# Kernel tuning notes

Measured on AMD Instinct MI355X. Metric: run time of the kernel, lower is better.

Reference implementation:

```python
import jax, jax.numpy as jnp
import numpy as np

BEV_H, BEV_W = 496, 432  # cfg.bevshape

def mish(x):
    return x * jnp.tanh(jax.nn.softplus(x))

def ln(x, g, b, eps=1e-5):
    m = jnp.mean(x, axis=-1, keepdims=True)
    v = jnp.mean((x - m) ** 2, axis=-1, keepdims=True)
    return (x - m) * jax.lax.rsqrt(v + eps) * g + b

def fel(x, W, g, b):
    # FELayer: Linear(bias=False) -> LayerNorm -> Mish
    return mish(ln(x @ W.T, g, b))

def setup_inputs() -> dict:
    key = jax.random.key(0)
    ks = iter(jax.random.split(key, 48))
    Nv, P, Cin, Cv, Nb = 16000, 32, 10, 64, 16000
    inp = {}
    inp['voxels'] = jax.random.normal(next(ks), (Nv, P, Cin), jnp.float32)
    inp['voxelmask'] = jax.random.bernoulli(next(ks), 0.7, (Nv, P, 1)).astype(jnp.float32)
    inp['bevsidx'] = jax.random.randint(next(ks), (Nb, 64), 0, Nv, dtype=jnp.int32)
    flat = jax.random.choice(next(ks), BEV_H * BEV_W, (Nb,), replace=False)
    inp['bevcoors'] = jnp.stack([flat // BEV_W, flat % BEV_W], axis=1).astype(jnp.int32)
    inp['bevmask'] = jax.random.bernoulli(next(ks), 0.8, (Nb, 1, 1)).astype(jnp.float32)
    def w(shape):
        return jax.random.normal(next(ks), shape, jnp.float32) * 0.05
    for i, cin in zip((1, 2, 3, 4), (Cin, Cv, Cv, Cv)):
        inp[f'vfe{i}_W'] = w((Cv, cin))
        inp[f'vfe{i}_g'] = jnp.ones((Cv,), jnp.float32)
        inp[f'vfe{i}_b'] = jnp.zeros((Cv,), jnp.float32)
    inp['bfe1_W'] = w((16, Cv, Cv));  inp['bfe1_g'] = jnp.ones((16, Cv));  inp['bfe1_b'] = jnp.zeros((16, Cv))
    inp['bfe2a_W'] = w((16, 8, Cv)); inp['bfe2a_g'] = jnp.ones((16, 8));  inp['bfe2a_b'] = jnp.zeros((16, 8))
    inp['bfe2b_W'] = w((16, 8, 32)); inp['bfe2b_g'] = jnp.ones((16, 8));  inp['bfe2b_b'] = jnp.zeros((16, 8))
    inp['bfe3_W'] = w((128, 128));   inp['bfe3_g'] = jnp.ones((128,));   inp['bfe3_b'] = jnp.zeros((128,))
    return inp

def reference(voxels, voxelmask, bevsidx, bevcoors, bevmask,
              vfe1_W, vfe1_g, vfe1_b, vfe2_W, vfe2_g, vfe2_b,
              vfe3_W, vfe3_g, vfe3_b, vfe4_W, vfe4_g, vfe4_b,
              bfe1_W, bfe1_g, bfe1_b, bfe2a_W, bfe2a_g, bfe2a_b,
              bfe2b_W, bfe2b_g, bfe2b_b, bfe3_W, bfe3_g, bfe3_b):
    # voxel feature encoder with masked residual
    x1 = fel(voxels, vfe1_W, vfe1_g, vfe1_b)            # [Nv, P, 64]
    x2 = fel(x1, vfe2_W, vfe2_g, vfe2_b) * voxelmask
    x3 = fel(x2, vfe3_W, vfe3_g, vfe3_b)
    x4 = fel(x3, vfe4_W, vfe4_g, vfe4_b) * voxelmask + x2
    voxelwise = jnp.max(x4, axis=1)                     # [Nv, 64]
    # gather 64 voxels per BEV cell
    bevs = voxelwise[bevsidx]                           # [Nb, 64 voxels, 64 ch]
    x0 = jnp.transpose(bevs, (0, 2, 1))                 # [Nb, 64 ch, 64 voxels]
    Nb = x0.shape[0]
    xg = x0.reshape(Nb, 16, 4, 64)                      # 16 branches of 4 channel-rows
    # bfe1_k (vectorized over the 16 branches) + bev mask
    h = mish(ln(jnp.einsum('ngpc,goc->ngpo', xg, bfe1_W), bfe1_g[:, None, :], bfe1_b[:, None, :]))
    h = h * bevmask[:, None]                            # bevmask [Nb,1,1] -> broadcast
    # bfe2_k: NormalFELayer(in_points=4, in=64, out=8)
    h = mish(ln(jnp.einsum('ngpc,goc->ngpo', h, bfe2a_W), bfe2a_g[:, None, :], bfe2a_b[:, None, :]))
    h = h.reshape(Nb, 16, 32)
    h = mish(ln(jnp.einsum('ngc,goc->ngo', h, bfe2b_W), bfe2b_g, bfe2b_b))  # [Nb,16,8]
    x17 = h.reshape(Nb, 128)                            # cat of 16 branches
    x18 = fel(x17, bfe3_W, bfe3_g, bfe3_b)
    x19 = fel(x18, bfe3_W, bfe3_g, bfe3_b) + x17        # same bfe3 applied twice + residual
    bevmap = jnp.zeros((BEV_H, BEV_W, 128), jnp.float32).at[bevcoors[:, 0], bevcoors[:, 1]].set(x19)
    return jnp.transpose(bevmap, (2, 1, 0))             # [128, W, H]
```

## Files before the change

kernel.cpp:

```cpp
#include <hip/hip_runtime.h>
#include <math.h>

constexpr int NV  = 16000;
constexpr int P   = 32;
constexpr int CIN = 10;
constexpr int CV  = 64;
constexpr int NB  = 16000;
constexpr int BEV_H = 496, BEV_W = 432;
constexpr int HW = BEV_H * BEV_W;
constexpr float EPS = 1e-5f;

typedef __attribute__((ext_vector_type(8))) short short8_t;
typedef __attribute__((ext_vector_type(4))) short short4_t;
typedef __attribute__((ext_vector_type(4))) float fx4;
typedef __attribute__((ext_vector_type(2))) float f32x2;

__device__ __forceinline__ float mish(float x) {
  float e = __expf(fminf(x, 15.f));
  float u = 1.f + e;
  float d = fmaf(u, u, 1.f);
  float r = __builtin_amdgcn_rcpf(d);
  return fmaf(-2.f * x, r, x);
}

__device__ __forceinline__ f32x2 mish2(f32x2 x) {
  f32x2 xc = __builtin_elementwise_min(x, (f32x2){15.f, 15.f});
  f32x2 e  = { __expf(xc[0]), __expf(xc[1]) };
  f32x2 u  = e + (f32x2){1.f, 1.f};
  f32x2 d  = __builtin_elementwise_fma(u, u, (f32x2){1.f, 1.f});
  f32x2 r  = { __builtin_amdgcn_rcpf(d[0]), __builtin_amdgcn_rcpf(d[1]) };
  f32x2 m2x = x * (f32x2){-2.f, -2.f};
  return __builtin_elementwise_fma(m2x, r, x);
}
__device__ __forceinline__ f32x2 ln2(f32x2 a, f32x2 rs, f32x2 msv, f32x2 go, f32x2 bo) {
  return __builtin_elementwise_fma(__builtin_elementwise_fma(a, rs, msv), go, bo);
}

__device__ __forceinline__ short f2bf(float f) {
  unsigned u = __builtin_bit_cast(unsigned, f);
  u += 0x7FFF + ((u >> 16) & 1);
  return (short)(u >> 16);
}
__device__ __forceinline__ float bf2f(short s) {
  unsigned u = ((unsigned)(unsigned short)s) << 16;
  return __builtin_bit_cast(float, u);
}
__device__ __forceinline__ short8_t pack8(const float* t) {
  short8_t s;
#pragma unroll
  for (int j = 0; j < 8; ++j) s[j] = f2bf(t[j]);
  return s;
}

__device__ __forceinline__ unsigned bfpair(float a, float b) {
  unsigned au = __builtin_bit_cast(unsigned, a) + 0x8000u;
  unsigned bu = __builtin_bit_cast(unsigned, b) + 0x8000u;
  return __builtin_amdgcn_perm(bu, au, 0x07060302u);
}
__device__ __forceinline__ unsigned hipack(float a, float b, float& la, float& lb) {
  unsigned ua = (__builtin_bit_cast(unsigned, a) + 0x8000u) & 0xFFFF0000u;
  unsigned ub = (__builtin_bit_cast(unsigned, b) + 0x8000u) & 0xFFFF0000u;
  la = a - __builtin_bit_cast(float, ua);
  lb = b - __builtin_bit_cast(float, ub);
  return __builtin_amdgcn_perm(ub, ua, 0x07060302u);
}

constexpr int VFE_BLOCKS  = NV / 16;
constexpr int PACK_BLOCKS = 208;

__global__ __launch_bounds__(512, 4) void vfe_pack_kernel(
    const float* __restrict__ voxels, const float* __restrict__ vmask,
    const float* __restrict__ W1, const float* __restrict__ g1, const float* __restrict__ b1,
    const float* __restrict__ W2, const float* __restrict__ g2, const float* __restrict__ b2,
    const float* __restrict__ W3, const float* __restrict__ g3, const float* __restrict__ b3,
    const float* __restrict__ W4, const float* __restrict__ g4, const float* __restrict__ b4,
    unsigned short* __restrict__ voxelwise,
    const float* __restrict__ bW1, const float* __restrict__ bW2a,
    const float* __restrict__ bW2b, const float* __restrict__ bW3,
    const int* __restrict__ bevcoors,
    short* __restrict__ w1h, short* __restrict__ w2ah, short* __restrict__ w2bh,
    short* __restrict__ w3h, short* __restrict__ w3l,
    int* __restrict__ invmap)
{
  __shared__ short wlds[28 * 512];
  __shared__ short actb[8][16 * 72];
  __shared__ float gblds[512];
  __shared__ unsigned short pairbuf[2][4][4][64];

  const int tid = threadIdx.x;

  if (blockIdx.x >= VFE_BLOCKS) {
    int i = (blockIdx.x - VFE_BLOCKS) * 512 + tid;
    if (i < NB) {
      int2 hw2 = *(const int2*)&bevcoors[i * 2];
      invmap[hw2.y * BEV_H + hw2.x] = i;
    }
    if (i < 65536) {
      w1h[i] = f2bf(bW1[i]);
    } else if (i < 81920) {
      int j = i - 65536;
      int g = j >> 10, o = (j >> 6) & 15, c = j & 63;
      float v = (o < 8) ? bW2a[(g * 8 + o) * 64 + c] : 0.f;
      w2ah[j] = f2bf(v);
    } else if (i < 90112) {
      int k = i - 81920;
      int g = k >> 9, o = (k >> 5) & 15, c = k & 31;
      float v = (o < 8) ? bW2b[(g * 8 + o) * 32 + c] : 0.f;
      w2bh[k] = f2bf(v);
    } else if (i < 106496) {
      int j = i - 90112;
      float v = bW3[j];
      short h = f2bf(v);
      w3h[j] = h; w3l[j] = f2bf(v - bf2f(h));
    }
    return;
  }

  const int lane = tid & 63;
  const int w    = tid >> 6;
  const int pair = w >> 1;
  const int h    = w & 1;
  const int p    = lane & 15;
  const int q    = lane >> 4;
  const int gw   = blockIdx.x * 4 + pair;

  {
    int region = tid >> 6, off = tid & 63;
    const float* src =
        region == 0 ? g1 : region == 1 ? b1 :
        region == 2 ? g2 : region == 3 ? b2 :
        region == 4 ? g3 : region == 5 ? b3 :
        region == 6 ? g4 : b4;
    gblds[tid] = src[off];
  }
  for (int s = w; s < 28; s += 8) {
    float t[8];
    if (s < 4) {
      const int f = s;
#pragma unroll
      for (int j = 0; j < 8; ++j) {
        int c = 8 * q + j;
        t[j] = (c < CIN) ? W1[(p + 16 * f) * CIN + c] : 0.f;
      }
    } else {
      const int l = (s - 4) >> 3, rem = (s - 4) & 7, ch = rem >> 2, f = rem & 3;
      const float* Wl = (l == 0) ? W2 : (l == 1) ? W3 : W4;
      const float* src = Wl + (p + 16 * f) * CV + 32 * ch + 8 * q;
#pragma unroll
      for (int j = 0; j < 8; ++j) t[j] = src[j];
    }
    *(short8_t*)&wlds[s * 512 + lane * 8] = pack8(t);
  }
  __syncthreads();

  short* mybuf = &actb[w][0];
  const fx4 zacc = {0.f, 0.f, 0.f, 0.f};
  const int srcLane = ((lane >> 2) & 3) * 16 + (((lane >> 4) & 3) << 2) + (lane & 3);

  for (int i = 0; i < 4; ++i) {
    const int v = gw * 4 + i;
    const int ptbase = v * 32 + h * 16;
    const float m = vmask[ptbase + p];
    const f32x2 mv = {m, m};
    f32x2 x2r2[8];
    float cur[16];

    {
      const float* xrow = voxels + (size_t)(ptbase + p) * CIN;
      float t[8] = {0.f, 0.f, 0.f, 0.f, 0.f, 0.f, 0.f, 0.f};
      if (q == 0) {
        float2 a = *(const float2*)(xrow + 0);
        float2 b = *(const float2*)(xrow + 2);
        float2 c = *(const float2*)(xrow + 4);
        float2 d = *(const float2*)(xrow + 6);
        t[0] = a.x; t[1] = a.y; t[2] = b.x; t[3] = b.y;
        t[4] = c.x; t[5] = c.y; t[6] = d.x; t[7] = d.y;
      } else if (q == 1) {
        float2 a = *(const float2*)(xrow + 8);
        t[0] = a.x; t[1] = a.y;
      }
      uint4 bu = make_uint4(bfpair(t[0], t[1]), bfpair(t[2], t[3]),
                            bfpair(t[4], t[5]), bfpair(t[6], t[7]));
      short8_t bfrag = __builtin_bit_cast(short8_t, bu);
      fx4 acc[4];
#pragma unroll
      for (int f = 0; f < 4; ++f) {
        short8_t af = *(short8_t*)&wlds[f * 512 + lane * 8];
        acc[f] = __builtin_amdgcn_mfma_f32_16x16x32_bf16(af, bfrag, zacc, 0, 0, 0);
      }
      f32x2 s1v = {0.f, 0.f}, s2v = {0.f, 0.f};
#pragma unroll
      for (int f = 0; f < 4; ++f) {
        f32x2 a01 = __builtin_shufflevector(acc[f], acc[f], 0, 1);
        f32x2 a23 = __builtin_shufflevector(acc[f], acc[f], 2, 3);
        s1v = s1v + a01 + a23;
        s2v = __builtin_elementwise_fma(a01, a01, s2v);
        s2v = __builtin_elementwise_fma(a23, a23, s2v);
      }
      float s1 = s1v[0] + s1v[1], s2 = s2v[0] + s2v[1];
      s1 += __shfl_xor(s1, 16); s1 += __shfl_xor(s1, 32);
      s2 += __shfl_xor(s2, 16); s2 += __shfl_xor(s2, 32);
      float mean = s1 * (1.f / 64.f);
      float rstd = rsqrtf(fmaf(-mean, mean, s2 * (1.f / 64.f)) + EPS);
      float ms = -mean * rstd;
      const f32x2 rs = {rstd, rstd}, msv = {ms, ms};
#pragma unroll
      for (int f = 0; f < 4; ++f) {
        float4 gv = *(const float4*)&gblds[16 * f + 4 * q];
        float4 bv = *(const float4*)&gblds[64 + 16 * f + 4 * q];
        f32x2 a01 = __builtin_shufflevector(acc[f], acc[f], 0, 1);
        f32x2 a23 = __builtin_shufflevector(acc[f], acc[f], 2, 3);
        f32x2 o01 = mish2(ln2(a01, rs, msv, (f32x2){gv.x, gv.y}, (f32x2){bv.x, bv.y}));
        f32x2 o23 = mish2(ln2(a23, rs, msv, (f32x2){gv.z, gv.w}, (f32x2){bv.z, bv.w}));
        *(uint2*)&mybuf[p * 72 + 4 * q + 16 * f] =
            make_uint2(bfpair(o01[0], o01[1]), bfpair(o23[0], o23[1]));
      }
    }

#pragma unroll 1
    for (int l = 0; l < 3; ++l) {
      short8_t bf0 = *(short8_t*)&mybuf[p * 72 + 8 * q];
      short8_t bf1 = *(short8_t*)&mybuf[p * 72 + 8 * q + 32];
      fx4 acc[4];
#pragma unroll
      for (int f = 0; f < 4; ++f) {
        short8_t a0 = *(short8_t*)&wlds[(4 + l * 8 + f) * 512 + lane * 8];
        short8_t a1 = *(short8_t*)&wlds[(4 + l * 8 + 4 + f) * 512 + lane * 8];
        fx4 a = __builtin_amdgcn_mfma_f32_16x16x32_bf16(a0, bf0, zacc, 0, 0, 0);
        acc[f] = __builtin_amdgcn_mfma_f32_16x16x32_bf16(a1, bf1, a, 0, 0, 0);
      }
      f32x2 s1v = {0.f, 0.f}, s2v = {0.f, 0.f};
#pragma unroll
      for (int f = 0; f < 4; ++f) {
        f32x2 a01 = __builtin_shufflevector(acc[f], acc[f], 0, 1);
        f32x2 a23 = __builtin_shufflevector(acc[f], acc[f], 2, 3);
        s1v = s1v + a01 + a23;
        s2v = __builtin_elementwise_fma(a01, a01, s2v);
        s2v = __builtin_elementwise_fma(a23, a23, s2v);
      }
      float s1 = s1v[0] + s1v[1], s2 = s2v[0] + s2v[1];
      s1 += __shfl_xor(s1, 16); s1 += __shfl_xor(s1, 32);
      s2 += __shfl_xor(s2, 16); s2 += __shfl_xor(s2, 32);
      float mean = s1 * (1.f / 64.f);
      float rstd = rsqrtf(fmaf(-mean, mean, s2 * (1.f / 64.f)) + EPS);
      float ms = -mean * rstd;
      const f32x2 rs = {rstd, rstd}, msv = {ms, ms};
      const int gbbase = (l + 1) * 128;
#pragma unroll
      for (int f = 0; f < 4; ++f) {
        float4 gv = *(const float4*)&gblds[gbbase + 16 * f + 4 * q];
        float4 bv = *(const float4*)&gblds[gbbase + 64 + 16 * f + 4 * q];
        f32x2 go01 = {gv.x, gv.y}, go23 = {gv.z, gv.w};
        f32x2 bo01 = {bv.x, bv.y}, bo23 = {bv.z, bv.w};
        f32x2 a01 = __builtin_shufflevector(acc[f], acc[f], 0, 1);
        f32x2 a23 = __builtin_shufflevector(acc[f], acc[f], 2, 3);
        if (l == 0) {
          f32x2 o01 = mish2(ln2(a01, rs, msv, go01, bo01)) * mv;
          f32x2 o23 = mish2(ln2(a23, rs, msv, go23, bo23)) * mv;
          x2r2[2 * f] = o01; x2r2[2 * f + 1] = o23;
          *(uint2*)&mybuf[p * 72 + 4 * q + 16 * f] =
              make_uint2(bfpair(o01[0], o01[1]), bfpair(o23[0], o23[1]));
        } else if (l == 1) {
          f32x2 o01 = mish2(ln2(a01, rs, msv, go01, bo01));
          f32x2 o23 = mish2(ln2(a23, rs, msv, go23, bo23));
          *(uint2*)&mybuf[p * 72 + 4 * q + 16 * f] =
              make_uint2(bfpair(o01[0], o01[1]), bfpair(o23[0], o23[1]));
        } else {
          f32x2 c01 = __builtin_elementwise_fma(
              mish2(ln2(a01, rs, msv, go01, bo01)), mv, x2r2[2 * f]);
          f32x2 c23 = __builtin_elementwise_fma(
              mish2(ln2(a23, rs, msv, go23, bo23)), mv, x2r2[2 * f + 1]);
          cur[f * 4 + 0] = c01[0]; cur[f * 4 + 1] = c01[1];
          cur[f * 4 + 2] = c23[0]; cur[f * 4 + 3] = c23[1];
        }
      }
    }

#pragma unroll
    for (int t = 0; t < 8; ++t) {
      float send = (lane & 8) ? cur[t] : cur[t + 8];
      float got  = __shfl_xor(send, 8);
      float mine = (lane & 8) ? cur[t + 8] : cur[t];
      cur[t] = fmaxf(mine, got);
    }
#pragma unroll
    for (int t = 0; t < 4; ++t) {
      float send = (lane & 4) ? cur[t] : cur[t + 4];
      float got  = __shfl_xor(send, 4);
      float mine = (lane & 4) ? cur[t + 4] : cur[t];
      cur[t] = fmaxf(mine, got);
    }
#pragma unroll
    for (int t = 0; t < 2; ++t) {
      float send = (lane & 2) ? cur[t] : cur[t + 2];
      float got  = __shfl_xor(send, 2);
      float mine = (lane & 2) ? cur[t + 2] : cur[t];
      cur[t] = fmaxf(mine, got);
    }
    {
      float send = (lane & 1) ? cur[0] : cur[1];
      float got  = __shfl_xor(send, 1);
      float mine = (lane & 1) ? cur[1] : cur[0];
      cur[0] = fmaxf(mine, got);
    }
    float hm = __shfl(cur[0], srcLane);
    unsigned hu = __builtin_bit_cast(unsigned, hm) + 0x8000u;
    pairbuf[h][pair][i][lane] = (unsigned short)(hu >> 16);
  }

  __syncthreads();

  if (h == 0) {
#pragma unroll
    for (int i = 0; i < 4; ++i) {
      const int v = gw * 4 + i;
      float a = bf2f((short)pairbuf[0][pair][i][lane]);
      float b = bf2f((short)pairbuf[1][pair][i][lane]);
      float vmaxv = fmaxf(a, b);
      voxelwise[v * 64 + lane] =
          (unsigned short)(__builtin_bit_cast(unsigned, vmaxv) >> 16);
    }
  }
}

constexpr int XS_CELL = 64 * 64 + 16;
constexpr int ACT_OFF = 4 * XS_CELL;
constexpr int ACT_WS  = 16 * 72;
constexpr int GB_OFF  = ACT_OFF + 8 * ACT_WS;
constexpr int GB_FLOATS = 2560;
constexpr int SMEM_SHORTS = GB_OFF + 2 * (GB_FLOATS + 4 * 132);

__device__ __forceinline__ uint2 gather_transpose(uint2 u2, int bit0, int bit1) {
  float a0 = __builtin_bit_cast(float, u2.x << 16);
  float a1 = __builtin_bit_cast(float, u2.x & 0xFFFF0000u);
  float a2 = __builtin_bit_cast(float, u2.y << 16);
  float a3 = __builtin_bit_cast(float, u2.y & 0xFFFF0000u);
  float gv0 = bit0 ? a0 : a1, gv1 = bit0 ? a2 : a3;
  float r0 = __shfl_xor(gv0, 4), r1 = __shfl_xor(gv1, 4);
  float c0 = bit0 ? r0 : a0, c1 = bit0 ? a1 : r0;
  float c2 = bit0 ? r1 : a2, c3 = bit0 ? a3 : r1;
  float h0 = bit1 ? c0 : c2, h1 = bit1 ? c1 : c3;
  float s0 = __shfl_xor(h0, 8), s1 = __shfl_xor(h1, 8);
  float d0 = bit1 ? s0 : c0, d1 = bit1 ? s1 : c1;
  float d2 = bit1 ? c2 : s0, d3 = bit1 ? c3 : s1;
  return make_uint2(bfpair(d0, d1), bfpair(d2, d3));
}

__global__ __launch_bounds__(512, 3) void bfe12_mfma10_kernel(
    const unsigned short* __restrict__ voxelwise, const int* __restrict__ bevsidx,
    const float* __restrict__ bevmask,
    const short* __restrict__ w1h,
    const float* __restrict__ g1, const float* __restrict__ b1,
    const short* __restrict__ w2ah,
    const float* __restrict__ g2a, const float* __restrict__ b2a,
    const short* __restrict__ w2bh,
    const float* __restrict__ g2b, const float* __restrict__ b2b,
    float* __restrict__ x17buf)
{
  __shared__ short sm[SMEM_SHORTS];
  float* gbf  = (float*)&sm[GB_OFF];
  float* x17f = gbf + GB_FLOATS;

  const int tid  = threadIdx.x;
  const int lane = tid & 63;
  const int w    = tid >> 6;
  const int r15  = lane & 15;
  const int q    = lane >> 4;
  const int cellbase = blockIdx.x * 4;

  const int chq   = lane & 3;
  const int v_loc = (lane >> 2) & 3;
  const int vblk  = lane >> 4;
  const int bit0  = v_loc & 1, bit1 = v_loc >> 1;
  const int gcell = w >> 1;
  const int vb0   = (w & 1) * 2;

  for (int k = tid; k < GB_FLOATS; k += 512) {
    float v;
    if (k < 1024)      v = g1[k];
    else if (k < 2048) v = b1[k - 1024];
    else if (k < 2176) v = g2a[k - 2048];
    else if (k < 2304) v = b2a[k - 2176];
    else if (k < 2432) v = g2b[k - 2304];
    else               v = b2b[k - 2432];
    gbf[k] = v;
  }

  int idxr[2];
#pragma unroll
  for (int vi = 0; vi < 2; ++vi)
    idxr[vi] = bevsidx[(cellbase + gcell) * 64 + 16 * (vb0 + vi) + 4 * vblk + v_loc];

  uint2 raw[2][4];
#pragma unroll
  for (int vi = 0; vi < 2; ++vi)
#pragma unroll
    for (int js = 0; js < 4; ++js)
      raw[vi][js] = *(const uint2*)(voxelwise + (size_t)idxr[vi] * 64 +
                                    16 * js + 4 * chq);

  short8_t W1f[2][2][4];
  short8_t W2af[2][2];
  short8_t W2bf[2];
#pragma unroll
  for (int j = 0; j < 2; ++j) {
    const int g = 8 * j + w;
#pragma unroll
    for (int c = 0; c < 2; ++c)
#pragma unroll
      for (int f = 0; f < 4; ++f) {
        int off = (g * 64 + r15 + 16 * f) * 64 + 32 * c + 8 * q;
        W1f[j][c][f] = *(const short8_t*)&w1h[off];
      }
#pragma unroll
    for (int c = 0; c < 2; ++c) {
      int off = (g * 16 + r15) * 64 + 32 * c + 8 * q;
      W2af[j][c] = *(const short8_t*)&w2ah[off];
    }
    {
      int off = (g * 16 + r15) * 32 + 8 * q;
      W2bf[j] = *(const short8_t*)&w2bh[off];
    }
  }

#pragma unroll
  for (int js = 0; js < 4; ++js)
#pragma unroll
    for (int vi = 0; vi < 2; ++vi) {
      uint2 packed = gather_transpose(raw[vi][js], bit0, bit1);
      const int vb    = vb0 + vi;
      const int ch    = 16 * js + 4 * chq + v_loc;
      const int chunk = (2 * vb + (vblk >> 1)) ^ (ch & 7);
      const int addr  = gcell * XS_CELL + ch * 64 + 8 * chunk + 4 * (vblk & 1);
      *(uint2*)&sm[addr] = packed;
    }

  __syncthreads();

  const fx4 zacc = {0.f, 0.f, 0.f, 0.f};
  short* acth = &sm[ACT_OFF + w * ACT_WS];
  short* h2h  = acth;
  const int cl = r15 >> 2, p = r15 & 3;
  const float bm = bevmask[cellbase + cl];
  const f32x2 bmv = {bm, bm};

#pragma unroll
  for (int j = 0; j < 2; ++j) {
    const int g = 8 * j + w;

    {
      const int ch    = 4 * g + p;
      const int sw    = ch & 7;
      const int xbase = cl * XS_CELL + ch * 64;
      short8_t x0 = *(short8_t*)&sm[xbase + 8 * (q ^ sw)];
      short8_t x1 = *(short8_t*)&sm[xbase + 8 * ((4 + q) ^ sw)];

      fx4 acc[4];
#pragma unroll
      for (int f = 0; f < 4; ++f) {
        fx4 a = __builtin_amdgcn_mfma_f32_16x16x32_bf16(W1f[j][0][f], x0, zacc, 0, 0, 0);
        acc[f] = __builtin_amdgcn_mfma_f32_16x16x32_bf16(W1f[j][1][f], x1, a, 0, 0, 0);
      }

      f32x2 s1v = {0.f, 0.f}, s2v = {0.f, 0.f};
#pragma unroll
      for (int f = 0; f < 4; ++f) {
        f32x2 a01 = __builtin_shufflevector(acc[f], acc[f], 0, 1);
        f32x2 a23 = __builtin_shufflevector(acc[f], acc[f], 2, 3);
        s1v = s1v + a01 + a23;
        s2v = __builtin_elementwise_fma(a01, a01, s2v);
        s2v = __builtin_elementwise_fma(a23, a23, s2v);
      }
      float s1 = s1v[0] + s1v[1], s2 = s2v[0] + s2v[1];
      s1 += __shfl_xor(s1, 16); s1 += __shfl_xor(s1, 32);
      s2 += __shfl_xor(s2, 16); s2 += __shfl_xor(s2, 32);
      float mean = s1 * (1.f / 64.f);
      float rstd = rsqrtf(fmaf(-mean, mean, s2 * (1.f / 64.f)) + EPS);
      float ms = -mean * rstd;
      const f32x2 rs = {rstd, rstd}, msv = {ms, ms};

#pragma unroll
      for (int f = 0; f < 4; ++f) {
        float4 gv = *(const float4*)&gbf[g * 64 + 16 * f + 4 * q];
        float4 bv = *(const float4*)&gbf[1024 + g * 64 + 16 * f + 4 * q];
        f32x2 a01 = __builtin_shufflevector(acc[f], acc[f], 0, 1);
        f32x2 a23 = __builtin_shufflevector(acc[f], acc[f], 2, 3);
        f32x2 o01 = mish2(ln2(a01, rs, msv, (f32x2){gv.x, gv.y}, (f32x2){bv.x, bv.y})) * bmv;
        f32x2 o23 = mish2(ln2(a23, rs, msv, (f32x2){gv.z, gv.w}, (f32x2){bv.z, bv.w})) * bmv;
        *(uint2*)&acth[r15 * 72 + 16 * f + 4 * q] =
            make_uint2(bfpair(o01[0], o01[1]), bfpair(o23[0], o23[1]));
      }

      short8_t a0 = *(short8_t*)&acth[r15 * 72 + 8 * q];
      short8_t a1 = *(short8_t*)&acth[r15 * 72 + 32 + 8 * q];

      if (lane < 60) *(uint2*)&h2h[160 + 8 * lane] = make_uint2(0u, 0u);

      fx4 a2 = __builtin_amdgcn_mfma_f32_16x16x32_bf16(W2af[j][0], a0, zacc, 0, 0, 0);
      a2 = __builtin_amdgcn_mfma_f32_16x16x32_bf16(W2af[j][1], a1, a2, 0, 0, 0);

      float sa = a2[0] + a2[1] + a2[2] + a2[3];
      float sb = fmaf(a2[0], a2[0], fmaf(a2[1], a2[1], fmaf(a2[2], a2[2], a2[3] * a2[3])));
      sa += __shfl_xor(sa, 16); sb += __shfl_xor(sb, 16);
      if (q < 2) {
        float mean2 = sa * 0.125f;
        float rstd2 = rsqrtf(fmaf(-mean2, mean2, sb * 0.125f) + EPS);
        float ms2 = -mean2 * rstd2;
        const f32x2 rs2 = {rstd2, rstd2}, ms2v = {ms2, ms2};
        float4 gv = *(const float4*)&gbf[2048 + g * 8 + 4 * q];
        float4 bv = *(const float4*)&gbf[2176 + g * 8 + 4 * q];
        f32x2 o01 = mish2(ln2((f32x2){a2[0], a2[1]}, rs2, ms2v,
                              (f32x2){gv.x, gv.y}, (f32x2){bv.x, bv.y}));
        f32x2 o23 = mish2(ln2((f32x2){a2[2], a2[3]}, rs2, ms2v,
                              (f32x2){gv.z, gv.w}, (f32x2){bv.z, bv.w}));
        *(uint2*)&h2h[cl * 40 + p * 8 + 4 * q] =
            make_uint2(bfpair(o01[0], o01[1]), bfpair(o23[0], o23[1]));
      }
    }

    {
      short8_t bh = *(short8_t*)&h2h[r15 * 40 + 8 * q];
      fx4 a3 = __builtin_amdgcn_mfma_f32_16x16x32_bf16(W2bf[j], bh, zacc, 0, 0, 0);

      float sa = a3[0] + a3[1] + a3[2] + a3[3];
      float sb = fmaf(a3[0], a3[0], fmaf(a3[1], a3[1], fmaf(a3[2], a3[2], a3[3] * a3[3])));
      sa += __shfl_xor(sa, 16); sb += __shfl_xor(sb, 16);
      if (q < 2 && r15 < 4) {
        float mean3 = sa * 0.125f;
        float rstd3 = rsqrtf(fmaf(-mean3, mean3, sb * 0.125f) + EPS);
        float ms3 = -mean3 * rstd3;
        const f32x2 rs3 = {rstd3, rstd3}, ms3v = {ms3, ms3};
        float4 gv = *(const float4*)&gbf[2304 + g * 8 + 4 * q];
        float4 bv = *(const float4*)&gbf[2432 + g * 8 + 4 * q];
        f32x2 o01 = mish2(ln2((f32x2){a3[0], a3[1]}, rs3, ms3v,
                              (f32x2){gv.x, gv.y}, (f32x2){bv.x, bv.y}));
        f32x2 o23 = mish2(ln2((f32x2){a3[2], a3[3]}, rs3, ms3v,
                              (f32x2){gv.z, gv.w}, (f32x2){bv.z, bv.w}));
        float4 outv = {o01[0], o01[1], o23[0], o23[1]};
        *(float4*)&x17f[r15 * 132 + g * 8 + 4 * q] = outv;
      }
    }
  }

  __syncthreads();
  if (tid < 128) {
    const int cell = tid >> 5;
    const int off  = (tid & 31) * 4;
    float4 vq = *(const float4*)&x17f[cell * 132 + off];
    *(float4*)&x17buf[(size_t)(cellbase + cell) * 128 + off] = vq;
  }
}

__global__ __launch_bounds__(64, 4) void bfe3_mfma5_kernel(
    const float* __restrict__ x17buf,
    const short* __restrict__ w3h, const short* __restrict__ w3l,
    const float* __restrict__ g3, const float* __restrict__ b3,
    float* __restrict__ x19c)
{
  __shared__ short xh18[16 * 136];
  __shared__ short xl18[16 * 136];

  const int tid  = threadIdx.x;
  const int lane = tid & 63;
  const int r15  = lane & 15;
  const int q    = lane >> 4;
  const int cell = blockIdx.x * 16 + r15;
  const float* xr = x17buf + (size_t)cell * 128;
  const fx4 zacc = {0.f, 0.f, 0.f, 0.f};

  short8_t xh[4], xl[4];
#pragma unroll
  for (int c = 0; c < 4; ++c) {
    const float* s = xr + 32 * c + 8 * q;
    float4 A = *(const float4*)s;
    float4 B = *(const float4*)(s + 4);
    float t[8] = {A.x, A.y, A.z, A.w, B.x, B.y, B.z, B.w};
    unsigned hu[4], lu[4];
#pragma unroll
    for (int jj = 0; jj < 4; ++jj) {
      float la, lb;
      hu[jj] = hipack(t[2 * jj], t[2 * jj + 1], la, lb);
      lu[jj] = bfpair(la, lb);
    }
    xh[c] = __builtin_bit_cast(short8_t, make_uint4(hu[0], hu[1], hu[2], hu[3]));
    xl[c] = __builtin_bit_cast(short8_t, make_uint4(lu[0], lu[1], lu[2], lu[3]));
  }

  fx4 acc[8];
#pragma unroll
  for (int f = 0; f < 8; ++f) {
    fx4 a = zacc;
#pragma unroll
    for (int c = 0; c < 4; ++c) {
      int off = (16 * f + r15) * 128 + 32 * c + 8 * q;
      short8_t Ah = *(const short8_t*)&w3h[off];
      short8_t Al = *(const short8_t*)&w3l[off];
      a = __builtin_amdgcn_mfma_f32_16x16x32_bf16(Ah, xh[c], a, 0, 0, 0);
      a = __builtin_amdgcn_mfma_f32_16x16x32_bf16(Ah, xl[c], a, 0, 0, 0);
      a = __builtin_amdgcn_mfma_f32_16x16x32_bf16(Al, xh[c], a, 0, 0, 0);
    }
    acc[f] = a;
  }
  {
    f32x2 s1v = {0.f, 0.f}, s2v = {0.f, 0.f};
#pragma unroll
    for (int f = 0; f < 8; ++f) {
      f32x2 a01 = __builtin_shufflevector(acc[f], acc[f], 0, 1);
      f32x2 a23 = __builtin_shufflevector(acc[f], acc[f], 2, 3);
      s1v = s1v + a01 + a23;
      s2v = __builtin_elementwise_fma(a01, a01, s2v);
      s2v = __builtin_elementwise_fma(a23, a23, s2v);
    }
    float s1 = s1v[0] + s1v[1], s2 = s2v[0] + s2v[1];
    s1 += __shfl_xor(s1, 16); s1 += __shfl_xor(s1, 32);
    s2 += __shfl_xor(s2, 16); s2 += __shfl_xor(s2, 32);
    float mean = s1 * (1.f / 128.f);
    float rstd = rsqrtf(fmaf(-mean, mean, s2 * (1.f / 128.f)) + EPS);
    float ms = -mean * rstd;
    const f32x2 rs = {rstd, rstd}, msv = {ms, ms};
#pragma unroll
    for (int f = 0; f < 8; ++f) {
      float4 gv = *(const float4*)(g3 + 16 * f + 4 * q);
      float4 bv = *(const float4*)(b3 + 16 * f + 4 * q);
      f32x2 a01 = __builtin_shufflevector(acc[f], acc[f], 0, 1);
      f32x2 a23 = __builtin_shufflevector(acc[f], acc[f], 2, 3);
      f32x2 o01 = mish2(ln2(a01, rs, msv, (f32x2){gv.x, gv.y}, (f32x2){bv.x, bv.y}));
      f32x2 o23 = mish2(ln2(a23, rs, msv, (f32x2){gv.z, gv.w}, (f32x2){bv.z, bv.w}));
      float la0, lb0, la1, lb1;
      unsigned h01 = hipack(o01[0], o01[1], la0, lb0);
      unsigned h23 = hipack(o23[0], o23[1], la1, lb1);
      *(uint2*)&xh18[r15 * 136 + 16 * f + 4 * q] = make_uint2(h01, h23);
      *(uint2*)&xl18[r15 * 136 + 16 * f + 4 * q] =
          make_uint2(bfpair(la0, lb0), bfpair(la1, lb1));
    }
  }

  short8_t yh[4], yl[4];
#pragma unroll
  for (int c = 0; c < 4; ++c) {
    yh[c] = *(short8_t*)&xh18[r15 * 136 + 32 * c + 8 * q];
    yl[c] = *(short8_t*)&xl18[r15 * 136 + 32 * c + 8 * q];
  }
#pragma unroll
  for (int f = 0; f < 8; ++f) {
    fx4 a = zacc;
#pragma unroll
    for (int c = 0; c < 4; ++c) {
      int off = (16 * f + r15) * 128 + 32 * c + 8 * q;
      short8_t Ah = *(const short8_t*)&w3h[off];
      short8_t Al = *(const short8_t*)&w3l[off];
      a = __builtin_amdgcn_mfma_f32_16x16x32_bf16(Ah, yh[c], a, 0, 0, 0);
      a = __builtin_amdgcn_mfma_f32_16x16x32_bf16(Ah, yl[c], a, 0, 0, 0);
      a = __builtin_amdgcn_mfma_f32_16x16x32_bf16(Al, yh[c], a, 0, 0, 0);
    }
    acc[f] = a;
  }
  {
    f32x2 s1v = {0.f, 0.f}, s2v = {0.f, 0.f};
#pragma unroll
    for (int f = 0; f < 8; ++f) {
      f32x2 a01 = __builtin_shufflevector(acc[f], acc[f], 0, 1);
      f32x2 a23 = __builtin_shufflevector(acc[f], acc[f], 2, 3);
      s1v = s1v + a01 + a23;
      s2v = __builtin_elementwise_fma(a01, a01, s2v);
      s2v = __builtin_elementwise_fma(a23, a23, s2v);
    }
    float s1 = s1v[0] + s1v[1], s2 = s2v[0] + s2v[1];
    s1 += __shfl_xor(s1, 16); s1 += __shfl_xor(s1, 32);
    s2 += __shfl_xor(s2, 16); s2 += __shfl_xor(s2, 32);
    float mean = s1 * (1.f / 128.f);
    float rstd = rsqrtf(fmaf(-mean, mean, s2 * (1.f / 128.f)) + EPS);
    float ms = -mean * rstd;
    const f32x2 rs = {rstd, rstd}, msv = {ms, ms};

#pragma unroll
    for (int f = 0; f < 8; ++f) {
      float4 gv = *(const float4*)(g3 + 16 * f + 4 * q);
      float4 bv = *(const float4*)(b3 + 16 * f + 4 * q);
      float4 R = *(const float4*)(xr + 16 * f + 4 * q);
      f32x2 a01 = __builtin_shufflevector(acc[f], acc[f], 0, 1);
      f32x2 a23 = __builtin_shufflevector(acc[f], acc[f], 2, 3);
      f32x2 o01 = mish2(ln2(a01, rs, msv, (f32x2){gv.x, gv.y}, (f32x2){bv.x, bv.y}))
                  + (f32x2){R.x, R.y};
      f32x2 o23 = mish2(ln2(a23, rs, msv, (f32x2){gv.z, gv.w}, (f32x2){bv.z, bv.w}))
                  + (f32x2){R.z, R.w};
      float4 ov = {o01[0], o01[1], o23[0], o23[1]};
      *(float4*)&x19c[(size_t)cell * 128 + 16 * f + 4 * q] = ov;
    }
  }
}

__global__ __launch_bounds__(256) void expand_kernel(
    const float* __restrict__ x19c, const int* __restrict__ invmap,
    float* __restrict__ out)
{
  __shared__ float tile[128][68];
  const int tid   = threadIdx.x;
  const int pbase = blockIdx.x * 64;
  const int r     = tid & 63;
  const int part  = tid >> 6;
  const int cell  = invmap[pbase + r];
  if (cell >= 0) {
    const float* src = x19c + (size_t)cell * 128 + part * 32;
#pragma unroll
    for (int k = 0; k < 8; ++k) {
      float4 v = *(const float4*)(src + 4 * k);
      tile[part * 32 + 4 * k + 0][r] = v.x;
      tile[part * 32 + 4 * k + 1][r] = v.y;
      tile[part * 32 + 4 * k + 2][r] = v.z;
      tile[part * 32 + 4 * k + 3][r] = v.w;
    }
  } else {
#pragma unroll
    for (int k = 0; k < 32; ++k) tile[part * 32 + k][r] = 0.f;
  }
  __syncthreads();
#pragma unroll
  for (int k = 0; k < 8; ++k) {
    int unit = k * 256 + tid;
    int c    = unit >> 4;
    int quad = unit & 15;
    float4 v = *(const float4*)&tile[c][quad * 4];
    *(float4*)&out[(size_t)c * HW + pbase + quad * 4] = v;
  }
}

extern "C" void kernel_launch(void* const* d_in, const int* in_sizes, int n_in,
                              void* d_out, int out_size, void* d_ws, size_t ws_size,
                              hipStream_t stream) {
  const float* voxels   = (const float*)d_in[0];
  const float* vmask    = (const float*)d_in[1];
  const int*   bevsidx  = (const int*)d_in[2];
  const int*   bevcoors = (const int*)d_in[3];
  const float* bevmask  = (const float*)d_in[4];
  const float* vfe1_W = (const float*)d_in[5];
  const float* vfe1_g = (const float*)d_in[6];
  const float* vfe1_b = (const float*)d_in[7];
  const float* vfe2_W = (const float*)d_in[8];
  const float* vfe2_g = (const float*)d_in[9];
  const float* vfe2_b = (const float*)d_in[10];
  const float* vfe3_W = (const float*)d_in[11];
  const float* vfe3_g = (const float*)d_in[12];
  const float* vfe3_b = (const float*)d_in[13];
  const float* vfe4_W = (const float*)d_in[14];
  const float* vfe4_g = (const float*)d_in[15];
  const float* vfe4_b = (const float*)d_in[16];
  const float* bfe1_W  = (const float*)d_in[17];
  const float* bfe1_g  = (const float*)d_in[18];
  const float* bfe1_b  = (const float*)d_in[19];
  const float* bfe2a_W = (const float*)d_in[20];
  const float* bfe2a_g = (const float*)d_in[21];
  const float* bfe2a_b = (const float*)d_in[22];
  const float* bfe2b_W = (const float*)d_in[23];
  const float* bfe2b_g = (const float*)d_in[24];
  const float* bfe2b_b = (const float*)d_in[25];
  const float* bfe3_W  = (const float*)d_in[26];
  const float* bfe3_g  = (const float*)d_in[27];
  const float* bfe3_b  = (const float*)d_in[28];

  unsigned short* voxelwise = (unsigned short*)d_ws;
  float* x17buf = (float*)(voxelwise + (size_t)NV * 64);
  float* x19c   = x17buf + (size_t)NB * 128;
  int*   invmap = (int*)(x19c + (size_t)NB * 128);
  short* wbase  = (short*)(invmap + HW);
  short* w1h  = wbase;
  short* w2ah = w1h + 65536;
  short* w2bh = w2ah + 16384;
  short* w3h  = w2bh + 8192;
  short* w3l  = w3h + 16384;
  float* out = (float*)d_out;

  hipMemsetAsync(invmap, 0xFF, (size_t)HW * sizeof(int), stream);

  vfe_pack_kernel<<<VFE_BLOCKS + PACK_BLOCKS, 512, 0, stream>>>(
      voxels, vmask,
      vfe1_W, vfe1_g, vfe1_b, vfe2_W, vfe2_g, vfe2_b,
      vfe3_W, vfe3_g, vfe3_b, vfe4_W, vfe4_g, vfe4_b,
      voxelwise,
      bfe1_W, bfe2a_W, bfe2b_W, bfe3_W, bevcoors,
      w1h, w2ah, w2bh, w3h, w3l, invmap);

  bfe12_mfma10_kernel<<<NB / 4, 512, 0, stream>>>(
      voxelwise, bevsidx, bevmask,
      w1h, bfe1_g, bfe1_b,
      w2ah, bfe2a_g, bfe2a_b,
      w2bh, bfe2b_g, bfe2b_b,
      x17buf);

  bfe3_mfma5_kernel<<<NB / 16, 64, 0, stream>>>(
      x17buf, w3h, w3l, bfe3_g, bfe3_b, x19c);

  expand_kernel<<<HW / 64, 256, 0, stream>>>(x19c, invmap, out);
}
```

Baseline: 395.0 us.

## Interleave both branch groups per wave in bfe12 to overlap MFMA chains

Restructures the per-wave loop over the two branch groups so that each stage (bfe1 MFMA, LayerNorm stats, Mish epilogue, bfe2a MFMA, bfe2b MFMA) runs for both groups back to back instead of finishing one group before starting the other. This exposes independent MFMA and reduction chains to hide latency. A second activation scratch region reuses the gathered-input LDS area, which is why a __syncthreads is added after the bfe1 MFMAs. It holds more accumulators live and so raises register pressure, which could hurt occupancy at the 512x3 launch bound.

```diff
diff --git a/kernel.cpp b/kernel.cpp
--- a/kernel.cpp
+++ b/kernel.cpp
@@ -346,7 +346,7 @@
   return make_uint2(bfpair(d0, d1), bfpair(d2, d3));
 }
 
-__global__ __launch_bounds__(512, 3) void bfe12_mfma10_kernel(
+__global__ __launch_bounds__(512, 3) void bfe12_mfma12_kernel(
     const unsigned short* __restrict__ voxelwise, const int* __restrict__ bevsidx,
     const float* __restrict__ bevmask,
     const short* __restrict__ w1h,
@@ -438,107 +438,142 @@
   __syncthreads();
 
   const fx4 zacc = {0.f, 0.f, 0.f, 0.f};
-  short* acth = &sm[ACT_OFF + w * ACT_WS];
-  short* h2h  = acth;
   const int cl = r15 >> 2, p = r15 & 3;
   const float bm = bevmask[cellbase + cl];
   const f32x2 bmv = {bm, bm};
-
+  short* const acthj0 = &sm[ACT_OFF + w * ACT_WS];
+  short* const acthj1 = &sm[w * ACT_WS];
+
+  fx4 acc1[2][4];
 #pragma unroll
   for (int j = 0; j < 2; ++j) {
     const int g = 8 * j + w;
-
-    {
-      const int ch    = 4 * g + p;
-      const int sw    = ch & 7;
-      const int xbase = cl * XS_CELL + ch * 64;
-      short8_t x0 = *(short8_t*)&sm[xbase + 8 * (q ^ sw)];
-      short8_t x1 = *(short8_t*)&sm[xbase + 8 * ((4 + q) ^ sw)];
-
-      fx4 acc[4];
-#pragma unroll
-      for (int f = 0; f < 4; ++f) {
-        fx4 a = __builtin_amdgcn_mfma_f32_16x16x32_bf16(W1f[j][0][f], x0, zacc, 0, 0, 0);
-        acc[f] = __builtin_amdgcn_mfma_f32_16x16x32_bf16(W1f[j][1][f], x1, a, 0, 0, 0);
-      }
-
-      f32x2 s1v = {0.f, 0.f}, s2v = {0.f, 0.f};
-#pragma unroll
-      for (int f = 0; f < 4; ++f) {
-        f32x2 a01 = __builtin_shufflevector(acc[f], acc[f], 0, 1);
-        f32x2 a23 = __builtin_shufflevector(acc[f], acc[f], 2, 3);
-        s1v = s1v + a01 + a23;
-        s2v = __builtin_elementwise_fma(a01, a01, s2v);
-        s2v = __builtin_elementwise_fma(a23, a23, s2v);
-      }
-      float s1 = s1v[0] + s1v[1], s2 = s2v[0] + s2v[1];
-      s1 += __shfl_xor(s1, 16); s1 += __shfl_xor(s1, 32);
-      s2 += __shfl_xor(s2, 16); s2 += __shfl_xor(s2, 32);
-      float mean = s1 * (1.f / 64.f);
-      float rstd = rsqrtf(fmaf(-mean, mean, s2 * (1.f / 64.f)) + EPS);
-      float ms = -mean * rstd;
-      const f32x2 rs = {rstd, rstd}, msv = {ms, ms};
-
-#pragma unroll
-      for (int f = 0; f < 4; ++f) {
-        float4 gv = *(const float4*)&gbf[g * 64 + 16 * f + 4 * q];
-        float4 bv = *(const float4*)&gbf[1024 + g * 64 + 16 * f + 4 * q];
-        f32x2 a01 = __builtin_shufflevector(acc[f], acc[f], 0, 1);
-        f32x2 a23 = __builtin_shufflevector(acc[f], acc[f], 2, 3);
-        f32x2 o01 = mish2(ln2(a01, rs, msv, (f32x2){gv.x, gv.y}, (f32x2){bv.x, bv.y})) * bmv;
-        f32x2 o23 = mish2(ln2(a23, rs, msv, (f32x2){gv.z, gv.w}, (f32x2){bv.z, bv.w})) * bmv;
-        *(uint2*)&acth[r15 * 72 + 16 * f + 4 * q] =
-            make_uint2(bfpair(o01[0], o01[1]), bfpair(o23[0], o23[1]));
-      }
-
-      short8_t a0 = *(short8_t*)&acth[r15 * 72 + 8 * q];
-      short8_t a1 = *(short8_t*)&acth[r15 * 72 + 32 + 8 * q];
-
-      if (lane < 60) *(uint2*)&h2h[160 + 8 * lane] = make_uint2(0u, 0u);
-
-      fx4 a2 = __builtin_amdgcn_mfma_f32_16x16x32_bf16(W2af[j][0], a0, zacc, 0, 0, 0);
-      a2 = __builtin_amdgcn_mfma_f32_16x16x32_bf16(W2af[j][1], a1, a2, 0, 0, 0);
-
-      float sa = a2[0] + a2[1] + a2[2] + a2[3];
-      float sb = fmaf(a2[0], a2[0], fmaf(a2[1], a2[1], fmaf(a2[2], a2[2], a2[3] * a2[3])));
-      sa += __shfl_xor(sa, 16); sb += __shfl_xor(sb, 16);
-      if (q < 2) {
-        float mean2 = sa * 0.125f;
-        float rstd2 = rsqrtf(fmaf(-mean2, mean2, sb * 0.125f) + EPS);
-        float ms2 = -mean2 * rstd2;
-        const f32x2 rs2 = {rstd2, rstd2}, ms2v = {ms2, ms2};
-        float4 gv = *(const float4*)&gbf[2048 + g * 8 + 4 * q];
-        float4 bv = *(const float4*)&gbf[2176 + g * 8 + 4 * q];
-        f32x2 o01 = mish2(ln2((f32x2){a2[0], a2[1]}, rs2, ms2v,
-                              (f32x2){gv.x, gv.y}, (f32x2){bv.x, bv.y}));
-        f32x2 o23 = mish2(ln2((f32x2){a2[2], a2[3]}, rs2, ms2v,
-                              (f32x2){gv.z, gv.w}, (f32x2){bv.z, bv.w}));
-        *(uint2*)&h2h[cl * 40 + p * 8 + 4 * q] =
-            make_uint2(bfpair(o01[0], o01[1]), bfpair(o23[0], o23[1]));
-      }
-    }
-
-    {
-      short8_t bh = *(short8_t*)&h2h[r15 * 40 + 8 * q];
-      fx4 a3 = __builtin_amdgcn_mfma_f32_16x16x32_bf16(W2bf[j], bh, zacc, 0, 0, 0);
-
-      float sa = a3[0] + a3[1] + a3[2] + a3[3];
-      float sb = fmaf(a3[0], a3[0], fmaf(a3[1], a3[1], fmaf(a3[2], a3[2], a3[3] * a3[3])));
-      sa += __shfl_xor(sa, 16); sb += __shfl_xor(sb, 16);
-      if (q < 2 && r15 < 4) {
-        float mean3 = sa * 0.125f;
-        float rstd3 = rsqrtf(fmaf(-mean3, mean3, sb * 0.125f) + EPS);
-        float ms3 = -mean3 * rstd3;
-        const f32x2 rs3 = {rstd3, rstd3}, ms3v = {ms3, ms3};
-        float4 gv = *(const float4*)&gbf[2304 + g * 8 + 4 * q];
-        float4 bv = *(const float4*)&gbf[2432 + g * 8 + 4 * q];
-        f32x2 o01 = mish2(ln2((f32x2){a3[0], a3[1]}, rs3, ms3v,
-                              (f32x2){gv.x, gv.y}, (f32x2){bv.x, bv.y}));
-        f32x2 o23 = mish2(ln2((f32x2){a3[2], a3[3]}, rs3, ms3v,
-                              (f32x2){gv.z, gv.w}, (f32x2){bv.z, bv.w}));
-        float4 outv = {o01[0], o01[1], o23[0], o23[1]};
-        *(float4*)&x17f[r15 * 132 + g * 8 + 4 * q] = outv;
-      }
+    const int ch    = 4 * g + p;
+    const int sw    = ch & 7;
+    const int xbase = cl * XS_CELL + ch * 64;
+    short8_t x0 = *(short8_t*)&sm[xbase + 8 * (q ^ sw)];
+    short8_t x1 = *(short8_t*)&sm[xbase + 8 * ((4 + q) ^ sw)];
+#pragma unroll
+    for (int f = 0; f < 4; ++f) {
+      fx4 a = __builtin_amdgcn_mfma_f32_16x16x32_bf16(W1f[j][0][f], x0, zacc, 0, 0, 0);
+      acc1[j][f] = __builtin_amdgcn_mfma_f32_16x16x32_bf16(W1f[j][1][f], x1, a, 0, 0, 0);
+    }
+  }
+
+  __syncthreads();
+
+  float rstd1[2], ms1[2];
+#pragma unroll
+  for (int j = 0; j < 2; ++j) {
+    f32x2 s1v = {0.f, 0.f}, s2v = {0.f, 0.f};
+#pragma unroll
+    for (int f = 0; f < 4; ++f) {
+      f32x2 a01 = __builtin_shufflevector(acc1[j][f], acc1[j][f], 0, 1);
+      f32x2 a23 = __builtin_shufflevector(acc1[j][f], acc1[j][f], 2, 3);
+      s1v = s1v + a01 + a23;
+      s2v = __builtin_elementwise_fma(a01, a01, s2v);
+      s2v = __builtin_elementwise_fma(a23, a23, s2v);
+    }
+    float s1 = s1v[0] + s1v[1], s2 = s2v[0] + s2v[1];
+    s1 += __shfl_xor(s1, 16); s1 += __shfl_xor(s1, 32);
+    s2 += __shfl_xor(s2, 16); s2 += __shfl_xor(s2, 32);
+    float mean = s1 * (1.f / 64.f);
+    rstd1[j] = rsqrtf(fmaf(-mean, mean, s2 * (1.f / 64.f)) + EPS);
+    ms1[j] = -mean * rstd1[j];
+  }
+
+#pragma unroll
+  for (int j = 0; j < 2; ++j) {
+    const int g = 8 * j + w;
+    short* const acth = j ? acthj1 : acthj0;
+    const f32x2 rs = {rstd1[j], rstd1[j]}, msv = {ms1[j], ms1[j]};
+#pragma unroll
+    for (int f = 0; f < 4; ++f) {
+      float4 gv = *(const float4*)&gbf[g * 64 + 16 * f + 4 * q];
+      float4 bv = *(const float4*)&gbf[1024 + g * 64 + 16 * f + 4 * q];
+      f32x2 a01 = __builtin_shufflevector(acc1[j][f], acc1[j][f], 0, 1);
+      f32x2 a23 = __builtin_shufflevector(acc1[j][f], acc1[j][f], 2, 3);
+      f32x2 o01 = mish2(ln2(a01, rs, msv, (f32x2){gv.x, gv.y}, (f32x2){bv.x, bv.y})) * bmv;
+      f32x2 o23 = mish2(ln2(a23, rs, msv, (f32x2){gv.z, gv.w}, (f32x2){bv.z, bv.w})) * bmv;
+      *(uint2*)&acth[r15 * 72 + 16 * f + 4 * q] =
+          make_uint2(bfpair(o01[0], o01[1]), bfpair(o23[0], o23[1]));
+    }
+  }
+
+  short8_t a0r0 = *(short8_t*)&acthj0[r15 * 72 + 8 * q];
+  short8_t a1r0 = *(short8_t*)&acthj0[r15 * 72 + 32 + 8 * q];
+  short8_t a0r1 = *(short8_t*)&acthj1[r15 * 72 + 8 * q];
+  short8_t a1r1 = *(short8_t*)&acthj1[r15 * 72 + 32 + 8 * q];
+  if (lane < 60) {
+    *(uint2*)&acthj0[160 + 8 * lane] = make_uint2(0u, 0u);
+    *(uint2*)&acthj1[160 + 8 * lane] = make_uint2(0u, 0u);
+  }
+  fx4 a2[2];
+  {
+    fx4 t0 = __builtin_amdgcn_mfma_f32_16x16x32_bf16(W2af[0][0], a0r0, zacc, 0, 0, 0);
+    fx4 t1 = __builtin_amdgcn_mfma_f32_16x16x32_bf16(W2af[1][0], a0r1, zacc, 0, 0, 0);
+    a2[0] = __builtin_amdgcn_mfma_f32_16x16x32_bf16(W2af[0][1], a1r0, t0, 0, 0, 0);
+    a2[1] = __builtin_amdgcn_mfma_f32_16x16x32_bf16(W2af[1][1], a1r1, t1, 0, 0, 0);
+  }
+
+  float rstd2[2], ms2[2];
+#pragma unroll
+  for (int j = 0; j < 2; ++j) {
+    float sa = a2[j][0] + a2[j][1] + a2[j][2] + a2[j][3];
+    float sb = fmaf(a2[j][0], a2[j][0], fmaf(a2[j][1], a2[j][1],
+               fmaf(a2[j][2], a2[j][2], a2[j][3] * a2[j][3])));
+    sa += __shfl_xor(sa, 16); sb += __shfl_xor(sb, 16);
+    float mean2 = sa * 0.125f;
+    rstd2[j] = rsqrtf(fmaf(-mean2, mean2, sb * 0.125f) + EPS);
+    ms2[j] = -mean2 * rstd2[j];
+  }
+  if (q < 2) {
+#pragma unroll
+    for (int j = 0; j < 2; ++j) {
+      const int g = 8 * j + w;
+      short* const h2h = j ? acthj1 : acthj0;
+      const f32x2 rs2 = {rstd2[j], rstd2[j]}, ms2v = {ms2[j], ms2[j]};
+      float4 gv = *(const float4*)&gbf[2048 + g * 8 + 4 * q];
+      float4 bv = *(const float4*)&gbf[2176 + g * 8 + 4 * q];
+      f32x2 o01 = mish2(ln2((f32x2){a2[j][0], a2[j][1]}, rs2, ms2v,
+                            (f32x2){gv.x, gv.y}, (f32x2){bv.x, bv.y}));
+      f32x2 o23 = mish2(ln2((f32x2){a2[j][2], a2[j][3]}, rs2, ms2v,
+                            (f32x2){gv.z, gv.w}, (f32x2){bv.z, bv.w}));
+      *(uint2*)&h2h[cl * 40 + p * 8 + 4 * q] =
+          make_uint2(bfpair(o01[0], o01[1]), bfpair(o23[0], o23[1]));
+    }
+  }
+
+  short8_t bhr0 = *(short8_t*)&acthj0[r15 * 40 + 8 * q];
+  short8_t bhr1 = *(short8_t*)&acthj1[r15 * 40 + 8 * q];
+  fx4 a3[2];
+  a3[0] = __builtin_amdgcn_mfma_f32_16x16x32_bf16(W2bf[0], bhr0, zacc, 0, 0, 0);
+  a3[1] = __builtin_amdgcn_mfma_f32_16x16x32_bf16(W2bf[1], bhr1, zacc, 0, 0, 0);
+
+  float rstd3[2], ms3[2];
+#pragma unroll
+  for (int j = 0; j < 2; ++j) {
+    float sa = a3[j][0] + a3[j][1] + a3[j][2] + a3[j][3];
+    float sb = fmaf(a3[j][0], a3[j][0], fmaf(a3[j][1], a3[j][1],
+               fmaf(a3[j][2], a3[j][2], a3[j][3] * a3[j][3])));
+    sa += __shfl_xor(sa, 16); sb += __shfl_xor(sb, 16);
+    float mean3 = sa * 0.125f;
+    rstd3[j] = rsqrtf(fmaf(-mean3, mean3, sb * 0.125f) + EPS);
+    ms3[j] = -mean3 * rstd3[j];
+  }
+  if (q < 2 && r15 < 4) {
+#pragma unroll
+    for (int j = 0; j < 2; ++j) {
+      const int g = 8 * j + w;
+      const f32x2 rs3 = {rstd3[j], rstd3[j]}, ms3v = {ms3[j], ms3[j]};
+      float4 gv = *(const float4*)&gbf[2304 + g * 8 + 4 * q];
+      float4 bv = *(const float4*)&gbf[2432 + g * 8 + 4 * q];
+      f32x2 o01 = mish2(ln2((f32x2){a3[j][0], a3[j][1]}, rs3, ms3v,
+                            (f32x2){gv.x, gv.y}, (f32x2){bv.x, bv.y}));
+      f32x2 o23 = mish2(ln2((f32x2){a3[j][2], a3[j][3]}, rs3, ms3v,
+                            (f32x2){gv.z, gv.w}, (f32x2){bv.z, bv.w}));
+      float4 outv = {o01[0], o01[1], o23[0], o23[1]};
+      *(float4*)&x17f[r15 * 132 + g * 8 + 4 * q] = outv;
     }
   }
 
@@ -780,7 +815,7 @@
       bfe1_W, bfe2a_W, bfe2b_W, bfe3_W, bevcoors,
       w1h, w2ah, w2bh, w3h, w3l, invmap);
 
-  bfe12_mfma10_kernel<<<NB / 4, 512, 0, stream>>>(
+  bfe12_mfma12_kernel<<<NB / 4, 512, 0, stream>>>(
       voxelwise, bevsidx, bevmask,
       w1h, bfe1_g, bfe1_b,
       w2ah, bfe2a_g, bfe2a_b,
```

New measurement: 458.1 us. 1.16x slower.
